# Kernel optimization log

Hardware: AMD Instinct MI355X
Metric: run time of the kernel (lower is better)

Reference implementation:

```python
import jax, jax.numpy as jnp
import numpy as np

B = 256        # graph pairs
MAX_SET = 64   # nodes per graph == max_set_size (padding is identity)
E = 512        # edges per graph
D = 128        # node_state_dim == av.filters_3
T = 64         # av.transform_dim
N_PROP = 5
N_TIME = 3
TEMP = 0.1
SINK_ITERS = 20
NG = 2 * B
N = NG * MAX_SET
TOT_E = NG * E


def sinkhorn(log_alpha):
    la = log_alpha / TEMP
    for _ in range(SINK_ITERS):
        la = la - jax.nn.logsumexp(la, axis=2, keepdims=True)
        la = la - jax.nn.logsumexp(la, axis=1, keepdims=True)
    return jnp.exp(la)


def setup_inputs() -> dict:
    key = jax.random.key(0)
    ks = jax.random.split(key, 32)

    def lin(k, i, o):
        return jax.random.normal(k, (i, o), jnp.float32) / np.sqrt(i).astype(np.float32)

    node_features = jax.random.normal(ks[0], (N, 32), jnp.float32)
    edge_features = jax.random.normal(ks[1], (TOT_E, 16), jnp.float32)
    offs = jnp.repeat(jnp.arange(NG, dtype=jnp.int32) * MAX_SET, E)
    from_idx = jax.random.randint(ks[2], (TOT_E,), 0, MAX_SET, jnp.int32) + offs
    to_idx = jax.random.randint(ks[3], (TOT_E,), 0, MAX_SET, jnp.int32) + offs
    return {
        "node_features": node_features, "edge_features": edge_features,
        "from_idx": from_idx, "to_idx": to_idx,
        "node_enc_w": lin(ks[4], 32, D), "node_enc_b": jnp.zeros((D,), jnp.float32),
        "edge_enc_w": lin(ks[5], 16, 64), "edge_enc_b": jnp.zeros((64,), jnp.float32),
        "mw1": lin(ks[6], 2 * D + 64, 2 * D), "mb1": jnp.zeros((2 * D,), jnp.float32),
        "mw2": lin(ks[7], 2 * D, D), "mb2": jnp.zeros((D,), jnp.float32),
        "nw1": lin(ks[8], 2 * D, 2 * D), "nb1": jnp.zeros((2 * D,), jnp.float32),
        "nw2": lin(ks[9], 2 * D, D), "nb2": jnp.zeros((D,), jnp.float32),
        "cw1": lin(ks[10], 2 * D, 2 * D), "cb1": jnp.zeros((2 * D,), jnp.float32),
        "cw2": lin(ks[11], 2 * D, D), "cb2": jnp.zeros((D,), jnp.float32),
        "t1w": lin(ks[12], D, T), "t1b": jnp.zeros((T,), jnp.float32),
        "t2w": lin(ks[13], T, T), "t2b": jnp.zeros((T,), jnp.float32),
    }


def reference(node_features, edge_features, from_idx, to_idx,
              node_enc_w, node_enc_b, edge_enc_w, edge_enc_b,
              mw1, mb1, mw2, mb2, nw1, nb1, nw2, nb2,
              cw1, cb1, cw2, cb2, t1w, t1b, t2w, t2b):
    # Encoder (GMN GraphEncoder: linear maps on raw node/edge features)
    h0 = node_features @ node_enc_w + node_enc_b          # [N, D]
    e0 = edge_features @ edge_enc_w + edge_enc_b          # [TOT_E, 64]
    store = jnp.zeros((N, D * (N_PROP + 1)), h0.dtype)    # node_feature_store
    plan = None
    for _t in range(N_TIME):
        h = h0
        parts = [jnp.zeros((N, D), h0.dtype)]             # slot 0 stays zero
        for p in range(1, N_PROP + 1):
            inter = store[:, (p - 1) * D: p * D]          # time_update_idx == 'k_t'
            comb = jax.nn.relu(jnp.concatenate([h, inter], 1) @ cw1 + cb1) @ cw2 + cb2
            # GraphPropLayer: gather -> message MLP -> segment_sum -> node update MLP
            msg_in = jnp.concatenate([comb[from_idx], comb[to_idx], e0], 1)
            messages = jax.nn.relu(msg_in @ mw1 + mb1) @ mw2 + mb2
            agg = jax.ops.segment_sum(messages, to_idx, num_segments=N)
            h = jax.nn.relu(jnp.concatenate([comb, agg], 1) @ nw1 + nb1) @ nw2 + nb2
            parts.append(h)
        store = jnp.concatenate(parts, 1)                 # [N, D*(K+1)]
        # split into padded query/corpus stacks (all graphs have MAX_SET nodes,
        # so F.pad and the size masks are identity here)
        s = store.reshape(NG, MAX_SET, -1)
        q, c = s[0::2], s[1::2]                           # [B, M, D*(K+1)]
        tq = jax.nn.relu(q[:, :, -D:] @ t1w + t1b) @ t2w + t2b
        tc = jax.nn.relu(c[:, :, -D:] @ t1w + t1b) @ t2w + t2b
        sim = jnp.einsum('bqt,bct->bqc', tq, tc)
        plan = sinkhorn(sim)                              # node transport plan [B,M,M]
        qfc = jnp.einsum('bqc,bcd->bqd', plan, c)
        cfq = jnp.einsum('bqc,bqd->bcd', plan, q)
        inter_feats = jnp.stack([qfc, cfq], 1)[:, :, :, D:].reshape(N, N_PROP * D)
        store = store.at[:, D:].set(inter_feats)
    return plan
```

## Files before the change

kernel.cpp:

```cpp
#include <hip/hip_runtime.h>
#include <hip/hip_bf16.h>

#define NNODES   32768
#define NGROUPS  512
#define EPG      512
#define ND       (32768l*128)

typedef __attribute__((ext_vector_type(4))) float f32x4;
typedef __attribute__((ext_vector_type(8))) short bf16x8;

__device__ __forceinline__ short f2bf(float x) {
  unsigned u = __float_as_uint(x);
  unsigned r = (u + 0x7FFF + ((u >> 16) & 1)) >> 16;
  return (short)r;
}
__device__ __forceinline__ float bf2f(short h) {
  return __uint_as_float(((unsigned)(unsigned short)h) << 16);
}
__device__ __forceinline__ void split3(float x, short* ph, short* pm, short* pl, long idx) {
  short h = f2bf(x); float r1 = x - bf2f(h);
  short m = f2bf(r1); float r2 = r1 - bf2f(m);
  ph[idx] = h; pm[idx] = m; pl[idx] = f2bf(r2);
}

__global__ void k_node_enc(const float* __restrict__ nf, const float* __restrict__ w,
                           const float* __restrict__ b, float* __restrict__ h0) {
  int idx = blockIdx.x * 256 + threadIdx.x;
  int row = idx >> 7, col = idx & 127;
  const float* x = nf + row * 32;
  float acc = b[col];
#pragma unroll
  for (int k = 0; k < 32; ++k) acc = fmaf(x[k], w[k * 128 + col], acc);
  h0[idx] = acc;
}

__global__ void k_prep(const float* __restrict__ eew, const float* __restrict__ eeb,
                       const float* __restrict__ mw1, const float* __restrict__ mb1,
                       const float* __restrict__ mb2, const float* __restrict__ nw1,
                       float* __restrict__ Wfold, float* __restrict__ bfold,
                       float* __restrict__ vbias) {
  const int c = threadIdx.x, b = blockIdx.x;
  if (b < 16) {
    float a = 0.f;
    for (int j = 0; j < 64; ++j) a = fmaf(eew[b * 64 + j], mw1[(256 + j) * 256 + c], a);
    Wfold[b * 256 + c] = a;
  } else if (b == 16) {
    float a = mb1[c];
    for (int j = 0; j < 64; ++j) a = fmaf(eeb[j], mw1[(256 + j) * 256 + c], a);
    bfold[c] = a;
  } else {
    float a = 0.f;
    for (int j = 0; j < 128; ++j) a = fmaf(mb2[j], nw1[(128 + j) * 256 + c], a);
    vbias[c] = a;
  }
}

__global__ void k_wsplit3(const float* __restrict__ W, int C, int Kd,
                          short* __restrict__ th, short* __restrict__ tm,
                          short* __restrict__ tl) {
  const int c = blockIdx.x;
  for (int k = threadIdx.x; k < Kd; k += 256) {
    float w = W[(long)k * C + c];
    split3(w, th, tm, tl, c * 256 + k);
  }
}

__global__ void k_csr(const int* __restrict__ from_idx, const int* __restrict__ to_idx,
                      const float* __restrict__ ef,
                      int* __restrict__ csr_f, int* __restrict__ rp_g,
                      float* __restrict__ efp, int* __restrict__ deg) {
  __shared__ int cnt[64], rps[65];
  __shared__ int tls[EPG], fls[EPG];
  __shared__ short ord[EPG];
  const int g = blockIdx.x, tid = threadIdx.x;
  const int be = g * EPG, bn = g * 64;
  if (tid < 64) cnt[tid] = 0;
  __syncthreads();
  for (int e = tid; e < EPG; e += 256) {
    int t = to_idx[be + e] - bn;
    tls[e] = t;
    fls[e] = from_idx[be + e] - bn;
    atomicAdd(&cnt[t], 1);
  }
  __syncthreads();
  if (tid == 0) {
    int s = 0;
    for (int i = 0; i < 64; ++i) { rps[i] = s; s += cnt[i]; }
    rps[64] = s;
  }
  __syncthreads();
  if (tid < 64) {
    int pos = rps[tid];
    for (int e = 0; e < EPG; ++e)
      if (tls[e] == tid) ord[pos++] = (short)e;
  }
  __syncthreads();
  for (int ec = tid; ec < EPG; ec += 256) {
    const int eo = ord[ec];
    csr_f[be + ec] = fls[eo];
    const float4* src = (const float4*)&ef[(long)(be + eo) * 16];
    float4* dst = (float4*)&efp[(long)(be + ec) * 16];
    dst[0] = src[0]; dst[1] = src[1]; dst[2] = src[2]; dst[3] = src[3];
  }
  if (tid < 65) rp_g[g * 65 + tid] = rps[tid];
  if (tid < 64) deg[bn + tid] = cnt[tid];
}

template<int KTOT, bool DEG, bool RPX0, bool WPOUT, bool AGG>
__global__ __launch_bounds__(256, 3)
void k_mlp2m(const float* __restrict__ x0,
             const short* __restrict__ x0h, const short* __restrict__ x0m,
             const short* __restrict__ x0l,
             const float* __restrict__ x1,
             const short* __restrict__ A2h, const short* __restrict__ A2m,
             const short* __restrict__ A2l,
             const short* __restrict__ W1h, const short* __restrict__ W1m,
             const short* __restrict__ W1l,
             const float* __restrict__ b1, const int* __restrict__ deg,
             const float* __restrict__ vbias,
             const short* __restrict__ W2h, const short* __restrict__ W2m,
             const short* __restrict__ W2l,
             const float* __restrict__ b2,
             float* __restrict__ out,
             short* __restrict__ outh, short* __restrict__ outm,
             short* __restrict__ outl) {
  __shared__ short xh[32 * 264];
  __shared__ short xm[32 * 264];
  __shared__ short xl[32 * 264];
  __shared__ int degs[32];
  const int tid = threadIdx.x;
  const long row0 = (long)blockIdx.x * 32;

  const int lane = tid & 63, wid = tid >> 6;
  const int lr = lane & 15;
  const int lk = (lane >> 4) * 8;
  const int rsub = (lane >> 4) * 4;

  if constexpr (AGG) {
    for (int i = tid; i < 2048; i += 256) {
      const int r = i >> 6, q = i & 63;
      float4 v = *(const float4*)&x1[(row0 + r) * 256 + q * 4];
      const int base = r * 264 + q * 4;
      split3(v.x, xh, xm, xl, base + 0);
      split3(v.y, xh, xm, xl, base + 1);
      split3(v.z, xh, xm, xl, base + 2);
      split3(v.w, xh, xm, xl, base + 3);
    }
    __syncthreads();

    f32x4 s0[2][2], s1[2][2];
#pragma unroll
    for (int fc = 0; fc < 2; ++fc)
#pragma unroll
      for (int fr = 0; fr < 2; ++fr) { s0[fr][fc] = {0.f,0.f,0.f,0.f}; s1[fr][fc] = {0.f,0.f,0.f,0.f}; }

#pragma unroll 2
    for (int ks = 0; ks < 4; ++ks) {
      const int k0 = ks * 32 + lk;
      bf16x8 ah[2], am[2], al[2];
#pragma unroll
      for (int fr = 0; fr < 2; ++fr) {
        const int ab = (fr * 16 + lr) * 264 + k0;
        ah[fr] = *(const bf16x8*)&xh[ab];
        am[fr] = *(const bf16x8*)&xm[ab];
        al[fr] = *(const bf16x8*)&xl[ab];
      }
#pragma unroll
      for (int fc = 0; fc < 2; ++fc) {
        const long wrow = (long)(wid * 32 + fc * 16 + lr) * 256 + k0;
        const bf16x8 bh = *(const bf16x8*)&A2h[wrow];
        const bf16x8 bm = *(const bf16x8*)&A2m[wrow];
        const bf16x8 bl = *(const bf16x8*)&A2l[wrow];
#pragma unroll
        for (int fr = 0; fr < 2; ++fr) {
          s0[fr][fc] = __builtin_amdgcn_mfma_f32_16x16x32_bf16(ah[fr], bh, s0[fr][fc], 0, 0, 0);
          s0[fr][fc] = __builtin_amdgcn_mfma_f32_16x16x32_bf16(ah[fr], bm, s0[fr][fc], 0, 0, 0);
          s0[fr][fc] = __builtin_amdgcn_mfma_f32_16x16x32_bf16(am[fr], bh, s0[fr][fc], 0, 0, 0);
          s0[fr][fc] = __builtin_amdgcn_mfma_f32_16x16x32_bf16(ah[fr], bl, s0[fr][fc], 0, 0, 0);
          s0[fr][fc] = __builtin_amdgcn_mfma_f32_16x16x32_bf16(am[fr], bm, s0[fr][fc], 0, 0, 0);
          s0[fr][fc] = __builtin_amdgcn_mfma_f32_16x16x32_bf16(al[fr], bh, s0[fr][fc], 0, 0, 0);
        }
      }
    }
#pragma unroll 2
    for (int ks = 4; ks < 8; ++ks) {
      const int k0 = ks * 32 + lk;
      bf16x8 ah[2], am[2], al[2];
#pragma unroll
      for (int fr = 0; fr < 2; ++fr) {
        const int ab = (fr * 16 + lr) * 264 + k0;
        ah[fr] = *(const bf16x8*)&xh[ab];
        am[fr] = *(const bf16x8*)&xm[ab];
        al[fr] = *(const bf16x8*)&xl[ab];
      }
#pragma unroll
      for (int fc = 0; fc < 2; ++fc) {
        const long wrow = (long)(wid * 32 + fc * 16 + lr) * 256 + k0;
        const bf16x8 bh = *(const bf16x8*)&A2h[wrow];
        const bf16x8 bm = *(const bf16x8*)&A2m[wrow];
        const bf16x8 bl = *(const bf16x8*)&A2l[wrow];
#pragma unroll
        for (int fr = 0; fr < 2; ++fr) {
          s1[fr][fc] = __builtin_amdgcn_mfma_f32_16x16x32_bf16(ah[fr], bh, s1[fr][fc], 0, 0, 0);
          s1[fr][fc] = __builtin_amdgcn_mfma_f32_16x16x32_bf16(ah[fr], bm, s1[fr][fc], 0, 0, 0);
          s1[fr][fc] = __builtin_amdgcn_mfma_f32_16x16x32_bf16(am[fr], bh, s1[fr][fc], 0, 0, 0);
          s1[fr][fc] = __builtin_amdgcn_mfma_f32_16x16x32_bf16(ah[fr], bl, s1[fr][fc], 0, 0, 0);
          s1[fr][fc] = __builtin_amdgcn_mfma_f32_16x16x32_bf16(am[fr], bm, s1[fr][fc], 0, 0, 0);
          s1[fr][fc] = __builtin_amdgcn_mfma_f32_16x16x32_bf16(al[fr], bh, s1[fr][fc], 0, 0, 0);
        }
      }
    }
    __syncthreads();

#pragma unroll
    for (int fr = 0; fr < 2; ++fr)
#pragma unroll
      for (int fc = 0; fc < 2; ++fc) {
        const int col = wid * 32 + fc * 16 + lr;
#pragma unroll
        for (int r = 0; r < 4; ++r) {
          const int row = fr * 16 + rsub + r;
          split3(s0[fr][fc][r] + s1[fr][fc][r], xh, xm, xl, row * 264 + 128 + col);
        }
      }
  }

  if constexpr (RPX0) {
    for (int i = tid; i < 32 * 16; i += 256) {
      const int r = i >> 4, q = i & 15;
      const long gb = (row0 + r) * 128 + q * 8;
      const int lb = r * 264 + q * 8;
      *(bf16x8*)&xh[lb] = *(const bf16x8*)&x0h[gb];
      *(bf16x8*)&xm[lb] = *(const bf16x8*)&x0m[gb];
      *(bf16x8*)&xl[lb] = *(const bf16x8*)&x0l[gb];
    }
  } else {
    for (int i = tid; i < 32 * 32; i += 256) {
      const int r = i >> 5, q = i & 31;
      float4 v = *(const float4*)&x0[(row0 + r) * 128 + q * 4];
      const int base = r * 264 + q * 4;
      split3(v.x, xh, xm, xl, base + 0);
      split3(v.y, xh, xm, xl, base + 1);
      split3(v.z, xh, xm, xl, base + 2);
      split3(v.w, xh, xm, xl, base + 3);
    }
  }
  if constexpr (KTOT == 256 && !AGG) {
    for (int i = tid; i < 32 * 32; i += 256) {
      const int r = i >> 5, q = i & 31;
      float4 v = *(const float4*)&x1[(row0 + r) * 128 + q * 4];
      const int base = r * 264 + 128 + q * 4;
      split3(v.x, xh, xm, xl, base + 0);
      split3(v.y, xh, xm, xl, base + 1);
      split3(v.z, xh, xm, xl, base + 2);
      split3(v.w, xh, xm, xl, base + 3);
    }
  }
  if constexpr (DEG) { if (tid < 32) degs[tid] = deg[row0 + tid]; }
  __syncthreads();

  f32x4 acc[2][4];
#pragma unroll
  for (int fc = 0; fc < 4; ++fc) {
    const int col = wid * 64 + fc * 16 + lr;
    const float bv = b1[col];
#pragma unroll
    for (int fr = 0; fr < 2; ++fr) acc[fr][fc] = {bv, bv, bv, bv};
    if constexpr (DEG) {
      const float vb = vbias[col];
#pragma unroll
      for (int fr = 0; fr < 2; ++fr)
#pragma unroll
        for (int r = 0; r < 4; ++r)
          acc[fr][fc][r] += (float)degs[fr * 16 + rsub + r] * vb;
    }
  }

#pragma unroll 2
  for (int ks = 0; ks < KTOT / 32; ++ks) {
    const int k0 = ks * 32 + lk;
    bf16x8 ah[2], am[2], al[2];
#pragma unroll
    for (int fr = 0; fr < 2; ++fr) {
      const int ab = (fr * 16 + lr) * 264 + k0;
      ah[fr] = *(const bf16x8*)&xh[ab];
      am[fr] = *(const bf16x8*)&xm[ab];
      al[fr] = *(const bf16x8*)&xl[ab];
    }
#pragma unroll
    for (int fc = 0; fc < 4; ++fc) {
      const long wrow = (long)(wid * 64 + fc * 16 + lr) * 256 + k0;
      const bf16x8 bh = *(const bf16x8*)&W1h[wrow];
      const bf16x8 bm = *(const bf16x8*)&W1m[wrow];
      const bf16x8 bl = *(const bf16x8*)&W1l[wrow];
#pragma unroll
      for (int fr = 0; fr < 2; ++fr) {
        acc[fr][fc] = __builtin_amdgcn_mfma_f32_16x16x32_bf16(ah[fr], bh, acc[fr][fc], 0, 0, 0);
        acc[fr][fc] = __builtin_amdgcn_mfma_f32_16x16x32_bf16(ah[fr], bm, acc[fr][fc], 0, 0, 0);
        acc[fr][fc] = __builtin_amdgcn_mfma_f32_16x16x32_bf16(am[fr], bh, acc[fr][fc], 0, 0, 0);
        acc[fr][fc] = __builtin_amdgcn_mfma_f32_16x16x32_bf16(ah[fr], bl, acc[fr][fc], 0, 0, 0);
        acc[fr][fc] = __builtin_amdgcn_mfma_f32_16x16x32_bf16(am[fr], bm, acc[fr][fc], 0, 0, 0);
        acc[fr][fc] = __builtin_amdgcn_mfma_f32_16x16x32_bf16(al[fr], bh, acc[fr][fc], 0, 0, 0);
      }
    }
  }
  __syncthreads();

#pragma unroll
  for (int fr = 0; fr < 2; ++fr)
#pragma unroll
    for (int fc = 0; fc < 4; ++fc) {
      const int col = wid * 64 + fc * 16 + lr;
#pragma unroll
      for (int r = 0; r < 4; ++r) {
        const int row = fr * 16 + rsub + r;
        float v = fmaxf(acc[fr][fc][r], 0.f);
        split3(v, xh, xm, xl, row * 264 + col);
      }
    }
  __syncthreads();

  f32x4 acc2[2][2];
#pragma unroll
  for (int fc = 0; fc < 2; ++fc) {
    const float bv = b2[wid * 32 + fc * 16 + lr];
#pragma unroll
    for (int fr = 0; fr < 2; ++fr) acc2[fr][fc] = {bv, bv, bv, bv};
  }
#pragma unroll 2
  for (int ks = 0; ks < 8; ++ks) {
    const int k0 = ks * 32 + lk;
    bf16x8 ah[2], am[2], al[2];
#pragma unroll
    for (int fr = 0; fr < 2; ++fr) {
      const int ab = (fr * 16 + lr) * 264 + k0;
      ah[fr] = *(const bf16x8*)&xh[ab];
      am[fr] = *(const bf16x8*)&xm[ab];
      al[fr] = *(const bf16x8*)&xl[ab];
    }
#pragma unroll
    for (int fc = 0; fc < 2; ++fc) {
      const long wrow = (long)(wid * 32 + fc * 16 + lr) * 256 + k0;
      const bf16x8 bh = *(const bf16x8*)&W2h[wrow];
      const bf16x8 bm = *(const bf16x8*)&W2m[wrow];
      const bf16x8 bl = *(const bf16x8*)&W2l[wrow];
#pragma unroll
      for (int fr = 0; fr < 2; ++fr) {
        acc2[fr][fc] = __builtin_amdgcn_mfma_f32_16x16x32_bf16(ah[fr], bh, acc2[fr][fc], 0, 0, 0);
        acc2[fr][fc] = __builtin_amdgcn_mfma_f32_16x16x32_bf16(ah[fr], bm, acc2[fr][fc], 0, 0, 0);
        acc2[fr][fc] = __builtin_amdgcn_mfma_f32_16x16x32_bf16(am[fr], bh, acc2[fr][fc], 0, 0, 0);
        acc2[fr][fc] = __builtin_amdgcn_mfma_f32_16x16x32_bf16(ah[fr], bl, acc2[fr][fc], 0, 0, 0);
        acc2[fr][fc] = __builtin_amdgcn_mfma_f32_16x16x32_bf16(am[fr], bm, acc2[fr][fc], 0, 0, 0);
        acc2[fr][fc] = __builtin_amdgcn_mfma_f32_16x16x32_bf16(al[fr], bh, acc2[fr][fc], 0, 0, 0);
      }
    }
  }
#pragma unroll
  for (int fr = 0; fr < 2; ++fr)
#pragma unroll
    for (int fc = 0; fc < 2; ++fc) {
      const int col = wid * 32 + fc * 16 + lr;
#pragma unroll
      for (int r = 0; r < 4; ++r) {
        const long gi = (row0 + fr * 16 + rsub + r) * 128 + col;
        if constexpr (WPOUT) {
          split3(acc2[fr][fc][r], outh, outm, outl, gi);
        } else {
          out[gi] = acc2[fr][fc][r];
        }
      }
    }
}

__global__ __launch_bounds__(256, 3)
void k_edgeb(const short* __restrict__ chp, const short* __restrict__ cmp,
             const short* __restrict__ clp,
             const float* __restrict__ efp,
             const short* __restrict__ m1h, const short* __restrict__ m1m,
             const short* __restrict__ m1l,
             const float* __restrict__ Wfold, const float* __restrict__ bfold,
             const int* __restrict__ csr_f, const int* __restrict__ rp_g,
             float* __restrict__ ag) {
  __shared__ __align__(16) float cAB[2 * 64 * 68];
  __shared__ short fl[EPG];
  __shared__ int rp[65];
  float* cA = cAB;
  float* cB = cAB + 64 * 68;

  const int tid = threadIdx.x;
  const int cb = blockIdx.x, g = blockIdx.y;
  const int be = g * EPG, bn = g * 64;
  const int col0 = cb * 64;

  for (int i = tid; i < EPG; i += 256) fl[i] = (short)csr_f[be + i];
  if (tid < 65) rp[tid] = rp_g[g * 65 + tid];

  const int lane = tid & 63, wid = tid >> 6;
  const int lr = lane & 15;
  const int lk = (lane >> 4) * 8;
  const int rsub = (lane >> 4) * 4;
  const int ng = tid >> 4, cg = tid & 15;
  const int n0 = ng * 4, cq = cg * 4;

  {
    const int isB = wid >> 1;
    const int cw = (wid & 1) * 32;
    const int wkof = isB * 128;
    float* dstC = isB ? cB : cA;
#pragma unroll 1
    for (int hf = 0; hf < 2; ++hf) {
      f32x4 c[2][2];
#pragma unroll
      for (int fr = 0; fr < 2; ++fr)
#pragma unroll
        for (int fc = 0; fc < 2; ++fc) c[fr][fc] = {0.f, 0.f, 0.f, 0.f};
      for (int ks = 0; ks < 4; ++ks) {
        const int k0 = ks * 32 + lk;
        bf16x8 ah[2], am[2], al[2];
#pragma unroll
        for (int fr = 0; fr < 2; ++fr) {
          const long ga = (long)(bn + (hf * 2 + fr) * 16 + lr) * 128 + k0;
          ah[fr] = *(const bf16x8*)&chp[ga];
          am[fr] = *(const bf16x8*)&cmp[ga];
          al[fr] = *(const bf16x8*)&clp[ga];
        }
#pragma unroll
        for (int fc = 0; fc < 2; ++fc) {
          const long wrow = (long)(col0 + cw + fc * 16 + lr) * 256 + wkof + k0;
          const bf16x8 bh = *(const bf16x8*)&m1h[wrow];
          const bf16x8 bm = *(const bf16x8*)&m1m[wrow];
          const bf16x8 bl = *(const bf16x8*)&m1l[wrow];
#pragma unroll
          for (int fr = 0; fr < 2; ++fr) {
            c[fr][fc] = __builtin_amdgcn_mfma_f32_16x16x32_bf16(ah[fr], bh, c[fr][fc], 0, 0, 0);
            c[fr][fc] = __builtin_amdgcn_mfma_f32_16x16x32_bf16(ah[fr], bm, c[fr][fc], 0, 0, 0);
            c[fr][fc] = __builtin_amdgcn_mfma_f32_16x16x32_bf16(am[fr], bh, c[fr][fc], 0, 0, 0);
            c[fr][fc] = __builtin_amdgcn_mfma_f32_16x16x32_bf16(ah[fr], bl, c[fr][fc], 0, 0, 0);
            c[fr][fc] = __builtin_amdgcn_mfma_f32_16x16x32_bf16(am[fr], bm, c[fr][fc], 0, 0, 0);
            c[fr][fc] = __builtin_amdgcn_mfma_f32_16x16x32_bf16(al[fr], bh, c[fr][fc], 0, 0, 0);
          }
        }
      }
#pragma unroll
      for (int fr = 0; fr < 2; ++fr)
#pragma unroll
        for (int fc = 0; fc < 2; ++fc) {
          const int col = cw + fc * 16 + lr;
#pragma unroll
          for (int r = 0; r < 4; ++r)
            dstC[((hf * 2 + fr) * 16 + rsub + r) * 68 + col] = c[fr][fc][r];
        }
    }
  }
  float4 Wf[16];
#pragma unroll
  for (int k = 0; k < 16; ++k) Wf[k] = *(const float4*)&Wfold[k * 256 + col0 + cq];
  const float4 bf = *(const float4*)&bfold[col0 + cq];
  __syncthreads();

#pragma unroll
  for (int i = 0; i < 4; ++i) {
    const int n = n0 + i;
    const float4 cBn = *(const float4*)&cB[n * 68 + cq];
    const int eEnd = rp[n + 1];
    float4 a0 = make_float4(0.f, 0.f, 0.f, 0.f);
    float4 a1 = make_float4(0.f, 0.f, 0.f, 0.f);
    float4 a2 = make_float4(0.f, 0.f, 0.f, 0.f);
    int e = rp[n];
    for (; e + 2 < eEnd; e += 3) {
      const int f0 = fl[e], f1 = fl[e + 1], f2 = fl[e + 2];
      const float* er0 = efp + (long)(be + e) * 16;
      const float* er1 = efp + (long)(be + e + 1) * 16;
      const float* er2 = efp + (long)(be + e + 2) * 16;
      float4 ea[4], eb[4], ec[4];
#pragma unroll
      for (int kq = 0; kq < 4; ++kq) {
        ea[kq] = ((const float4*)er0)[kq];
        eb[kq] = ((const float4*)er1)[kq];
        ec[kq] = ((const float4*)er2)[kq];
      }
      float4 h0 = bf, h1 = bf, h2 = bf;
#pragma unroll
      for (int kq = 0; kq < 4; ++kq) {
        const float ev0[4] = {ea[kq].x, ea[kq].y, ea[kq].z, ea[kq].w};
        const float ev1[4] = {eb[kq].x, eb[kq].y, eb[kq].z, eb[kq].w};
        const float ev2[4] = {ec[kq].x, ec[kq].y, ec[kq].z, ec[kq].w};
#pragma unroll
        for (int s = 0; s < 4; ++s) {
          const float4 w = Wf[kq * 4 + s];
          h0.x = fmaf(ev0[s], w.x, h0.x); h0.y = fmaf(ev0[s], w.y, h0.y);
          h0.z = fmaf(ev0[s], w.z, h0.z); h0.w = fmaf(ev0[s], w.w, h0.w);
          h1.x = fmaf(ev1[s], w.x, h1.x); h1.y = fmaf(ev1[s], w.y, h1.y);
          h1.z = fmaf(ev1[s], w.z, h1.z); h1.w = fmaf(ev1[s], w.w, h1.w);
          h2.x = fmaf(ev2[s], w.x, h2.x); h2.y = fmaf(ev2[s], w.y, h2.y);
          h2.z = fmaf(ev2[s], w.z, h2.z); h2.w = fmaf(ev2[s], w.w, h2.w);
        }
      }
      const float4 va0 = *(const float4*)&cA[f0 * 68 + cq];
      const float4 va1 = *(const float4*)&cA[f1 * 68 + cq];
      const float4 va2 = *(const float4*)&cA[f2 * 68 + cq];
      a0.x += fmaxf(h0.x + va0.x + cBn.x, 0.f);
      a0.y += fmaxf(h0.y + va0.y + cBn.y, 0.f);
      a0.z += fmaxf(h0.z + va0.z + cBn.z, 0.f);
      a0.w += fmaxf(h0.w + va0.w + cBn.w, 0.f);
      a1.x += fmaxf(h1.x + va1.x + cBn.x, 0.f);
      a1.y += fmaxf(h1.y + va1.y + cBn.y, 0.f);
      a1.z += fmaxf(h1.z + va1.z + cBn.z, 0.f);
      a1.w += fmaxf(h1.w + va1.w + cBn.w, 0.f);
      a2.x += fmaxf(h2.x + va2.x + cBn.x, 0.f);
      a2.y += fmaxf(h2.y + va2.y + cBn.y, 0.f);
      a2.z += fmaxf(h2.z + va2.z + cBn.z, 0.f);
      a2.w += fmaxf(h2.w + va2.w + cBn.w, 0.f);
    }
    for (; e < eEnd; ++e) {
      const int f = fl[e];
      const float* er = efp + (long)(be + e) * 16;
      float4 h = bf;
#pragma unroll
      for (int kq = 0; kq < 4; ++kq) {
        const float4 e4 = ((const float4*)er)[kq];
        const float ev[4] = {e4.x, e4.y, e4.z, e4.w};
#pragma unroll
        for (int s = 0; s < 4; ++s) {
          const float4 w = Wf[kq * 4 + s];
          h.x = fmaf(ev[s], w.x, h.x); h.y = fmaf(ev[s], w.y, h.y);
          h.z = fmaf(ev[s], w.z, h.z); h.w = fmaf(ev[s], w.w, h.w);
        }
      }
      const float4 va = *(const float4*)&cA[f * 68 + cq];
      a0.x += fmaxf(h.x + va.x + cBn.x, 0.f);
      a0.y += fmaxf(h.y + va.y + cBn.y, 0.f);
      a0.z += fmaxf(h.z + va.z + cBn.z, 0.f);
      a0.w += fmaxf(h.w + va.w + cBn.w, 0.f);
    }
    a0.x += a1.x; a0.y += a1.y; a0.z += a1.z; a0.w += a1.w;
    a0.x += a2.x; a0.y += a2.y; a0.z += a2.z; a0.w += a2.w;
    *(float4*)&ag[(long)(bn + n) * 256 + col0 + cq] = a0;
  }
}

__global__ void k_tfeat(const float* __restrict__ x,
                        const float* __restrict__ t1w, const float* __restrict__ t1b,
                        const float* __restrict__ t2w, const float* __restrict__ t2b,
                        float* __restrict__ tf) {
  __shared__ float xs[4][128];
  __shared__ float ys[4][64];
  const int tid = threadIdx.x;
  const long row0 = (long)blockIdx.x * 4;
  for (int i = tid; i < 512; i += 256)
    xs[i >> 7][i & 127] = x[(row0 + (i >> 7)) * 128 + (i & 127)];
  __syncthreads();
  const int r = tid >> 6, c = tid & 63;
  float acc = t1b[c];
#pragma unroll 4
  for (int k = 0; k < 128; ++k) acc = fmaf(xs[r][k], t1w[k * 64 + c], acc);
  ys[r][c] = fmaxf(acc, 0.f);
  __syncthreads();
  float a2 = t2b[c];
#pragma unroll 4
  for (int k = 0; k < 64; ++k) a2 = fmaf(ys[r][k], t2w[k * 64 + c], a2);
  tf[(row0 + r) * 64 + c] = a2;
}

__global__ void k_sim(const float* __restrict__ tf, float* __restrict__ sim) {
  const int b = blockIdx.x, tid = threadIdx.x;
  __shared__ float tq[64][65];
  __shared__ float tcs[64][65];
  for (int i = tid; i < 4096; i += 256) {
    tq[i >> 6][i & 63]  = tf[(long)b * 8192 + i];
    tcs[i >> 6][i & 63] = tf[(long)b * 8192 + 4096 + i];
  }
  __syncthreads();
  const int m = tid >> 2, j0 = (tid & 3) * 16;
#pragma unroll
  for (int j = 0; j < 16; ++j) {
    float a = 0.f;
#pragma unroll 4
    for (int k = 0; k < 64; ++k) a = fmaf(tq[m][k], tcs[j0 + j][k], a);
    sim[(long)b * 4096 + m * 64 + j0 + j] = a;
  }
}

__global__ void k_sink(float* __restrict__ sim, float* __restrict__ outp) {
  const int b = blockIdx.x, tid = threadIdx.x;
  __shared__ float la[64][65];
  const float C = 14.426950408889634f;
  for (int i = tid; i < 4096; i += 256)
    la[i >> 6][i & 63] = sim[(long)b * 4096 + i] * C;
  __syncthreads();
  const int r4 = tid >> 2, l4 = tid & 3;
  for (int it = 0; it < 20; ++it) {
    {
      float m = -3.4e38f;
#pragma unroll
      for (int i = 0; i < 16; ++i) m = fmaxf(m, la[r4][l4 + 4 * i]);
      m = fmaxf(m, __shfl_xor(m, 1)); m = fmaxf(m, __shfl_xor(m, 2));
      float s = 0.f;
#pragma unroll
      for (int i = 0; i < 16; ++i) s += exp2f(la[r4][l4 + 4 * i] - m);
      s += __shfl_xor(s, 1); s += __shfl_xor(s, 2);
      const float lse = m + log2f(s);
#pragma unroll
      for (int i = 0; i < 16; ++i) la[r4][l4 + 4 * i] -= lse;
    }
    __syncthreads();
    {
      float m = -3.4e38f;
#pragma unroll
      for (int i = 0; i < 16; ++i) m = fmaxf(m, la[l4 + 4 * i][r4]);
      m = fmaxf(m, __shfl_xor(m, 1)); m = fmaxf(m, __shfl_xor(m, 2));
      float s = 0.f;
#pragma unroll
      for (int i = 0; i < 16; ++i) s += exp2f(la[l4 + 4 * i][r4] - m);
      s += __shfl_xor(s, 1); s += __shfl_xor(s, 2);
      const float lse = m + log2f(s);
#pragma unroll
      for (int i = 0; i < 16; ++i) la[l4 + 4 * i][r4] -= lse;
    }
    __syncthreads();
  }
  for (int i = tid; i < 4096; i += 256) {
    const float v = exp2f(la[i >> 6][i & 63]);
    outp[(long)b * 4096 + i] = v;
    sim[(long)b * 4096 + i] = v;
  }
}

__global__ void k_mix(const float* __restrict__ plan, const float* __restrict__ src,
                      float* __restrict__ dst) {
  const int b = blockIdx.x, tid = threadIdx.x;
  __shared__ float pl[64][65];
  __shared__ float qs[64][128];
  __shared__ float cs[64][128];
  const long qbase = (long)(2 * b) * 64, cbase = qbase + 64;
  for (int i = tid; i < 4096; i += 256) pl[i >> 6][i & 63] = plan[(long)b * 4096 + i];
  for (int i = tid; i < 8192; i += 256) {
    qs[i >> 7][i & 127] = src[qbase * 128 + i];
    cs[i >> 7][i & 127] = src[cbase * 128 + i];
  }
  __syncthreads();
  const int d = tid & 127, m0 = (tid >> 7) * 32;
  for (int m = m0; m < m0 + 32; ++m) {
    float a = 0.f;
#pragma unroll 4
    for (int j = 0; j < 64; ++j) a = fmaf(pl[m][j], cs[j][d], a);
    dst[(qbase + m) * 128 + d] = a;
  }
  for (int j = m0; j < m0 + 32; ++j) {
    float a = 0.f;
#pragma unroll 4
    for (int m = 0; m < 64; ++m) a = fmaf(pl[m][j], qs[m][d], a);
    dst[(cbase + j) * 128 + d] = a;
  }
}

extern "C" void kernel_launch(void* const* d_in, const int* in_sizes, int n_in,
                              void* d_out, int out_size, void* d_ws, size_t ws_size,
                              hipStream_t stream) {
  const float* nf  = (const float*)d_in[0];
  const float* ef  = (const float*)d_in[1];
  const int* from_idx = (const int*)d_in[2];
  const int* to_idx   = (const int*)d_in[3];
  const float* new_w = (const float*)d_in[4];
  const float* new_b = (const float*)d_in[5];
  const float* eew = (const float*)d_in[6];
  const float* eeb = (const float*)d_in[7];
  const float* mw1 = (const float*)d_in[8];
  const float* mb1 = (const float*)d_in[9];
  const float* mw2 = (const float*)d_in[10];
  const float* mb2 = (const float*)d_in[11];
  const float* nw1 = (const float*)d_in[12];
  const float* nb1 = (const float*)d_in[13];
  const float* nw2 = (const float*)d_in[14];
  const float* nb2 = (const float*)d_in[15];
  const float* cw1 = (const float*)d_in[16];
  const float* cb1 = (const float*)d_in[17];
  const float* cw2 = (const float*)d_in[18];
  const float* cb2 = (const float*)d_in[19];
  const float* t1w = (const float*)d_in[20];
  const float* t1b = (const float*)d_in[21];
  const float* t2w = (const float*)d_in[22];
  const float* t2b = (const float*)d_in[23];

  float* W = (float*)d_ws;
  float* h0     = W;
  float* aggM0  = h0 + ND;
  float* ag     = aggM0 + ND;
  float* parts  = ag + 2 * ND;
  float* efp    = parts + 5 * ND;
  float* Wfold  = efp + 262144l * 16;
  float* bfold  = Wfold + 4096;
  float* vbias  = bfold + 256;
  int*   deg    = (int*)(vbias + 256);
  int*   csr_f  = deg + 32768;
  int*   rp_g   = csr_f + 262144;
  short* cw1t_h = (short*)(rp_g + 33280);
  short* cw1t_m = cw1t_h + 65536;
  short* cw1t_l = cw1t_m + 65536;
  short* nw1t_h = cw1t_l + 65536;
  short* nw1t_m = nw1t_h + 65536;
  short* nw1t_l = nw1t_m + 65536;
  short* cw2t_h = nw1t_l + 65536;
  short* cw2t_m = cw2t_h + 32768;
  short* cw2t_l = cw2t_m + 32768;
  short* nw2t_h = cw2t_l + 32768;
  short* nw2t_m = nw2t_h + 32768;
  short* nw2t_l = nw2t_m + 32768;
  short* m1t_h  = nw2t_l + 32768;
  short* m1t_m  = m1t_h + 65536;
  short* m1t_l  = m1t_m + 65536;
  short* m2t_h  = m1t_l + 65536;
  short* m2t_m  = m2t_h + 32768;
  short* m2t_l  = m2t_m + 32768;
  short* chp    = m2t_l + 32768;
  short* cmp    = chp + 32768l * 128;
  short* clp    = cmp + 32768l * 128;
  float* tf     = aggM0;
  float* sim    = aggM0 + 2097152;
  float* outp   = (float*)d_out;

  k_prep<<<18, 256, 0, stream>>>(eew, eeb, mw1, mb1, mb2, nw1, Wfold, bfold, vbias);
  k_csr<<<512, 256, 0, stream>>>(from_idx, to_idx, ef, csr_f, rp_g, efp, deg);
  k_wsplit3<<<256, 256, 0, stream>>>(cw1, 256, 256, cw1t_h, cw1t_m, cw1t_l);
  k_wsplit3<<<256, 256, 0, stream>>>(nw1, 256, 256, nw1t_h, nw1t_m, nw1t_l);
  k_wsplit3<<<128, 256, 0, stream>>>(cw2, 128, 256, cw2t_h, cw2t_m, cw2t_l);
  k_wsplit3<<<128, 256, 0, stream>>>(nw2, 128, 256, nw2t_h, nw2t_m, nw2t_l);
  k_wsplit3<<<256, 256, 0, stream>>>(mw1, 256, 256, m1t_h, m1t_m, m1t_l);
  k_wsplit3<<<128, 256, 0, stream>>>(mw2, 128, 256, m2t_h, m2t_m, m2t_l);
  k_node_enc<<<16384, 256, 0, stream>>>(nf, new_w, new_b, h0);

  for (int t = 0; t < 3; ++t) {
    const float* hprev = h0;
    for (int p = 1; p <= 5; ++p) {
      if (t > 0 && p > 1)
        k_mlp2m<256, false, false, true, false><<<1024, 256, 0, stream>>>(
            hprev, nullptr, nullptr, nullptr,
            parts + (long)(p - 1) * ND, nullptr, nullptr, nullptr,
            cw1t_h, cw1t_m, cw1t_l, cb1, nullptr, nullptr,
            cw2t_h, cw2t_m, cw2t_l, cb2, nullptr, chp, cmp, clp);
      else
        k_mlp2m<128, false, false, true, false><<<1024, 256, 0, stream>>>(
            hprev, nullptr, nullptr, nullptr, nullptr, nullptr, nullptr, nullptr,
            cw1t_h, cw1t_m, cw1t_l, cb1, nullptr, nullptr,
            cw2t_h, cw2t_m, cw2t_l, cb2, nullptr, chp, cmp, clp);
      k_edgeb<<<dim3(4, 512), 256, 0, stream>>>(chp, cmp, clp, efp,
                                                m1t_h, m1t_m, m1t_l,
                                                Wfold, bfold, csr_f, rp_g, ag);
      float* hnew = parts + (long)(p - 1) * ND;
      k_mlp2m<256, true, true, false, true><<<1024, 256, 0, stream>>>(
          nullptr, chp, cmp, clp, ag, m2t_h, m2t_m, m2t_l,
          nw1t_h, nw1t_m, nw1t_l, nb1, deg, vbias,
          nw2t_h, nw2t_m, nw2t_l, nb2, hnew, nullptr, nullptr, nullptr);
      hprev = hnew;
    }
    k_tfeat<<<8192, 256, 0, stream>>>(parts + 4 * ND, t1w, t1b, t2w, t2b, tf);
    k_sim<<<256, 256, 0, stream>>>(tf, sim);
    k_sink<<<256, 256, 0, stream>>>(sim, outp);
    if (t < 2) {
      for (int pi = 3; pi >= 0; --pi)
        k_mix<<<256, 256, 0, stream>>>(sim, parts + (long)pi * ND, parts + (long)(pi + 1) * ND);
    }
  }
}
```

Before: 5.539 ms.

## Fuse transform, similarity and Sinkhorn into one kernel; merge four mix launches

The transform MLP, similarity einsum and Sinkhorn normalization now run in a single per-pair kernel, so the tf and sim intermediates stay in shared memory instead of going through global memory. The four per-layer mix launches become one kernel that loads the plan once and loops over the layers. This removes launches and global round trips. In exchange the transform MLP now runs on only 256 blocks, with 32 serial steps per block instead of 8192 parallel blocks, which lowers parallelism for that stage.

```diff
diff --git a/kernel.cpp b/kernel.cpp
--- a/kernel.cpp
+++ b/kernel.cpp
@@ -539,57 +539,52 @@
   }
 }
 
-__global__ void k_tfeat(const float* __restrict__ x,
-                        const float* __restrict__ t1w, const float* __restrict__ t1b,
-                        const float* __restrict__ t2w, const float* __restrict__ t2b,
-                        float* __restrict__ tf) {
+__global__ void k_pair(const float* __restrict__ x,
+                       const float* __restrict__ t1w, const float* __restrict__ t1b,
+                       const float* __restrict__ t2w, const float* __restrict__ t2b,
+                       float* __restrict__ sim, float* __restrict__ outp) {
+  const int b = blockIdx.x, tid = threadIdx.x;
   __shared__ float xs[4][128];
   __shared__ float ys[4][64];
-  const int tid = threadIdx.x;
-  const long row0 = (long)blockIdx.x * 4;
-  for (int i = tid; i < 512; i += 256)
-    xs[i >> 7][i & 127] = x[(row0 + (i >> 7)) * 128 + (i & 127)];
-  __syncthreads();
-  const int r = tid >> 6, c = tid & 63;
-  float acc = t1b[c];
-#pragma unroll 4
-  for (int k = 0; k < 128; ++k) acc = fmaf(xs[r][k], t1w[k * 64 + c], acc);
-  ys[r][c] = fmaxf(acc, 0.f);
-  __syncthreads();
-  float a2 = t2b[c];
-#pragma unroll 4
-  for (int k = 0; k < 64; ++k) a2 = fmaf(ys[r][k], t2w[k * 64 + c], a2);
-  tf[(row0 + r) * 64 + c] = a2;
-}
-
-__global__ void k_sim(const float* __restrict__ tf, float* __restrict__ sim) {
-  const int b = blockIdx.x, tid = threadIdx.x;
   __shared__ float tq[64][65];
   __shared__ float tcs[64][65];
-  for (int i = tid; i < 4096; i += 256) {
-    tq[i >> 6][i & 63]  = tf[(long)b * 8192 + i];
-    tcs[i >> 6][i & 63] = tf[(long)b * 8192 + 4096 + i];
-  }
-  __syncthreads();
-  const int m = tid >> 2, j0 = (tid & 3) * 16;
-#pragma unroll
-  for (int j = 0; j < 16; ++j) {
-    float a = 0.f;
+  __shared__ float la[64][65];
+  const long rbase = (long)b * 128;
+
+  for (int it = 0; it < 32; ++it) {
+    const long row0 = rbase + it * 4;
+    for (int i = tid; i < 512; i += 256)
+      xs[i >> 7][i & 127] = x[(row0 + (i >> 7)) * 128 + (i & 127)];
+    __syncthreads();
+    const int r = tid >> 6, c = tid & 63;
+    float acc = t1b[c];
 #pragma unroll 4
-    for (int k = 0; k < 64; ++k) a = fmaf(tq[m][k], tcs[j0 + j][k], a);
-    sim[(long)b * 4096 + m * 64 + j0 + j] = a;
-  }
-}
-
-__global__ void k_sink(float* __restrict__ sim, float* __restrict__ outp) {
-  const int b = blockIdx.x, tid = threadIdx.x;
-  __shared__ float la[64][65];
+    for (int k = 0; k < 128; ++k) acc = fmaf(xs[r][k], t1w[k * 64 + c], acc);
+    ys[r][c] = fmaxf(acc, 0.f);
+    __syncthreads();
+    float a2 = t2b[c];
+#pragma unroll 4
+    for (int k = 0; k < 64; ++k) a2 = fmaf(ys[r][k], t2w[k * 64 + c], a2);
+    const int rr = it * 4 + r;
+    if (rr < 64) tq[rr][c] = a2; else tcs[rr - 64][c] = a2;
+    __syncthreads();
+  }
+
   const float C = 14.426950408889634f;
-  for (int i = tid; i < 4096; i += 256)
-    la[i >> 6][i & 63] = sim[(long)b * 4096 + i] * C;
-  __syncthreads();
+  {
+    const int m = tid >> 2, j0 = (tid & 3) * 16;
+#pragma unroll
+    for (int j = 0; j < 16; ++j) {
+      float a = 0.f;
+#pragma unroll 4
+      for (int k = 0; k < 64; ++k) a = fmaf(tq[m][k], tcs[j0 + j][k], a);
+      la[m][j0 + j] = a * C;
+    }
+  }
+  __syncthreads();
+
   const int r4 = tid >> 2, l4 = tid & 3;
-  for (int it = 0; it < 20; ++it) {
+  for (int itn = 0; itn < 20; ++itn) {
     {
       float m = -3.4e38f;
 #pragma unroll
@@ -626,31 +621,39 @@
   }
 }
 
-__global__ void k_mix(const float* __restrict__ plan, const float* __restrict__ src,
-                      float* __restrict__ dst) {
+__global__ void k_mix4(const float* __restrict__ plan, float* __restrict__ parts) {
   const int b = blockIdx.x, tid = threadIdx.x;
   __shared__ float pl[64][65];
   __shared__ float qs[64][128];
   __shared__ float cs[64][128];
   const long qbase = (long)(2 * b) * 64, cbase = qbase + 64;
+
   for (int i = tid; i < 4096; i += 256) pl[i >> 6][i & 63] = plan[(long)b * 4096 + i];
-  for (int i = tid; i < 8192; i += 256) {
-    qs[i >> 7][i & 127] = src[qbase * 128 + i];
-    cs[i >> 7][i & 127] = src[cbase * 128 + i];
-  }
-  __syncthreads();
-  const int d = tid & 127, m0 = (tid >> 7) * 32;
-  for (int m = m0; m < m0 + 32; ++m) {
-    float a = 0.f;
+  __syncthreads();
+
+#pragma unroll 1
+  for (int pi = 3; pi >= 0; --pi) {
+    const float* src = parts + (long)pi * ND;
+    float* dst = parts + (long)(pi + 1) * ND;
+    for (int i = tid; i < 8192; i += 256) {
+      qs[i >> 7][i & 127] = src[qbase * 128 + i];
+      cs[i >> 7][i & 127] = src[cbase * 128 + i];
+    }
+    __syncthreads();
+    const int d = tid & 127, m0 = (tid >> 7) * 32;
+    for (int m = m0; m < m0 + 32; ++m) {
+      float a = 0.f;
 #pragma unroll 4
-    for (int j = 0; j < 64; ++j) a = fmaf(pl[m][j], cs[j][d], a);
-    dst[(qbase + m) * 128 + d] = a;
-  }
-  for (int j = m0; j < m0 + 32; ++j) {
-    float a = 0.f;
+      for (int j = 0; j < 64; ++j) a = fmaf(pl[m][j], cs[j][d], a);
+      dst[(qbase + m) * 128 + d] = a;
+    }
+    for (int j = m0; j < m0 + 32; ++j) {
+      float a = 0.f;
 #pragma unroll 4
-    for (int m = 0; m < 64; ++m) a = fmaf(pl[m][j], qs[m][d], a);
-    dst[(cbase + j) * 128 + d] = a;
+      for (int m = 0; m < 64; ++m) a = fmaf(pl[m][j], qs[m][d], a);
+      dst[(cbase + j) * 128 + d] = a;
+    }
+    __syncthreads();
   }
 }
 
@@ -715,8 +718,7 @@
   short* chp    = m2t_l + 32768;
   short* cmp    = chp + 32768l * 128;
   short* clp    = cmp + 32768l * 128;
-  float* tf     = aggM0;
-  float* sim    = aggM0 + 2097152;
+  float* sim    = aggM0;
   float* outp   = (float*)d_out;
 
   k_prep<<<18, 256, 0, stream>>>(eew, eeb, mw1, mb1, mb2, nw1, Wfold, bfold, vbias);
@@ -753,12 +755,7 @@
           nw2t_h, nw2t_m, nw2t_l, nb2, hnew, nullptr, nullptr, nullptr);
       hprev = hnew;
     }
-    k_tfeat<<<8192, 256, 0, stream>>>(parts + 4 * ND, t1w, t1b, t2w, t2b, tf);
-    k_sim<<<256, 256, 0, stream>>>(tf, sim);
-    k_sink<<<256, 256, 0, stream>>>(sim, outp);
-    if (t < 2) {
-      for (int pi = 3; pi >= 0; --pi)
-        k_mix<<<256, 256, 0, stream>>>(sim, parts + (long)pi * ND, parts + (long)(pi + 1) * ND);
-    }
-  }
-}
+    k_pair<<<256, 256, 0, stream>>>(parts + 4 * ND, t1w, t1b, t2w, t2b, sim, outp);
+    if (t < 2) k_mix4<<<256, 256, 0, stream>>>(sim, parts);
+  }
+}
```

Result: slower. 6.250 ms (+12.8%).
